# Kernel optimization log

Measured on AMD Instinct MI355X. Metric: run time of the kernel, lower is better.

The kernel has to match this reference:

```python
import jax, jax.numpy as jnp
import numpy as np

MASK_PROPORTION = 0.5
NEG_BIG = -99999999.0


def setup_inputs() -> dict:
    key = jax.random.key(0)
    k_x, k_w1, k_b1, k_w2, k_b2 = jax.random.split(key, 5)
    B, T, D, H = 32, 4096, 1024, 256
    x = jax.random.normal(k_x, (B, T, D), dtype=jnp.float32)
    s1 = 1.0 / np.sqrt(D)
    s2 = 1.0 / np.sqrt(H)
    W1 = jax.random.uniform(k_w1, (D, H), minval=-s1, maxval=s1, dtype=jnp.float32)
    b1 = jax.random.uniform(k_b1, (H,), minval=-s1, maxval=s1, dtype=jnp.float32)
    W2 = jax.random.uniform(k_w2, (H, 1), minval=-s2, maxval=s2, dtype=jnp.float32)
    b2 = jax.random.uniform(k_b2, (1,), minval=-s2, maxval=s2, dtype=jnp.float32)
    return {"x": x, "W1": W1, "b1": b1, "W2": W2, "b2": b2}


def reference(x, W1, b1, W2, b2):
    # e: [B, T, 1] attention scores from small MLP
    h = jnp.tanh(jnp.einsum("btd,dh->bth", x, W1) + b1)
    e = jnp.einsum("bth,ho->bto", h, W2) + b2  # [B, T, 1]

    T = e.shape[1]
    threshold_index = int(T * MASK_PROPORTION)
    sorted_e = jnp.sort(e, axis=1)
    threshold_value = sorted_e[:, threshold_index]          # [B, 1]
    # mask: +1 where e < threshold (kept), NEG_BIG where e >= threshold
    mask = jnp.where(e >= threshold_value[:, None, :], NEG_BIG, 1.0)
    e = e + mask
    beta = jax.nn.softmax(e, axis=1)                        # [B, T, 1]
    # bmm(beta^T, x) -> [B, 1, D], permute -> [B, D, 1], unsqueeze -> [B, D, 1, 1]
    out = jnp.einsum("bto,btd->bd", beta, x)
    return out[:, :, None, None]
```

## Files before the change

kernel.cpp:

```cpp
#include <hip/hip_runtime.h>
#include <hip/hip_bf16.h>
#include <math.h>

#define B_   32
#define T_   4096
#define D_   1024
#define H_   256
#define KTH  2048
#define SC   32
#define BM   128
#define BKE  32
#define NTE  (D_/BKE)
#define ABUF (BM*BKE)
#define BBUF (H_*BKE)
#define EPSB 4.0e-3f
#define MAXBAND 256
#define RB   4

typedef __attribute__((ext_vector_type(8))) short short8;
typedef __attribute__((ext_vector_type(4))) float f32x4;

#define FENCE4() asm volatile("s_waitcnt vmcnt(4) lgkmcnt(0)" ::: "memory")
#define FENCE0() asm volatile("s_waitcnt vmcnt(0) lgkmcnt(0)" ::: "memory")
#define BARRIER() __builtin_amdgcn_s_barrier()
#define SCHED()  __builtin_amdgcn_sched_barrier(0)
#define GLL(src, dst) __builtin_amdgcn_global_load_lds( \
    (const __attribute__((address_space(1))) unsigned int*)(src), \
    (__attribute__((address_space(3))) unsigned int*)(dst), 16, 0, 0)

__device__ inline unsigned f2s(float f) {
    unsigned u = __float_as_uint(f);
    return (u & 0x80000000u) ? ~u : (u | 0x80000000u);
}
__device__ inline float s2f(unsigned s) {
    unsigned x = (s & 0x80000000u) ? (s & 0x7fffffffu) : ~s;
    return __uint_as_float(x);
}
__device__ inline unsigned f2bf_rne(float f) {
    unsigned u = __float_as_uint(f);
    return (u + 0x7FFFu + ((u >> 16) & 1u)) >> 16;
}
__device__ inline unsigned pk2(float a, float b) {
    return f2bf_rne(a) | (f2bf_rne(b) << 16);
}
__device__ inline int block_sum_i(int v, int* sb, int tid) {
    #pragma unroll
    for (int o = 32; o; o >>= 1) v += __shfl_down(v, o);
    __syncthreads();
    if ((tid & 63) == 0) sb[tid >> 6] = v;
    __syncthreads();
    return sb[0] + sb[1] + sb[2] + sb[3];
}
__device__ inline float block_max_f(float v, float* sb, int tid) {
    #pragma unroll
    for (int o = 32; o; o >>= 1) v = fmaxf(v, __shfl_down(v, o));
    __syncthreads();
    if ((tid & 63) == 0) sb[tid >> 6] = v;
    __syncthreads();
    return fmaxf(fmaxf(sb[0], sb[1]), fmaxf(sb[2], sb[3]));
}
__device__ inline float block_sum_f(float v, float* sb, int tid) {
    #pragma unroll
    for (int o = 32; o; o >>= 1) v += __shfl_down(v, o);
    __syncthreads();
    if ((tid & 63) == 0) sb[tid >> 6] = v;
    __syncthreads();
    return sb[0] + sb[1] + sb[2] + sb[3];
}

__global__ __launch_bounds__(256) void k_w1t(const float* __restrict__ W1,
                                             ushort* __restrict__ Whi) {
    __shared__ float tile[32][33];
    const int kb = blockIdx.x * 32, nb = blockIdx.y * 32;
    const int tx = threadIdx.x & 31, ty = threadIdx.x >> 5;
    #pragma unroll
    for (int i = 0; i < 4; i++)
        tile[ty + 8*i][tx] = W1[(long)(kb + ty + 8*i) * H_ + nb + tx];
    __syncthreads();
    #pragma unroll
    for (int i = 0; i < 4; i++) {
        long o = (long)(nb + ty + 8*i) * D_ + kb + tx;
        Whi[o] = (ushort)f2bf_rne(tile[tx][ty + 8*i]);
    }
}

__global__ __launch_bounds__(512, 4) void k_e_mfma(
    const float* __restrict__ x,
    const ushort* __restrict__ Whi,
    const float* __restrict__ b1, const float* __restrict__ W2,
    const float* __restrict__ b2, float* __restrict__ e_out)
{
    __shared__ ushort sA[2][ABUF];
    __shared__ ushort sB[3][BBUF];
    __shared__ float  sRed[4][BM];

    const int tid  = threadIdx.x;
    const int lane = tid & 63;
    const int wv   = tid >> 6;
    const int wm   = wv >> 2, wn = wv & 3;
    const int l15  = lane & 15, lg = lane >> 4;
    const long row0 = (long)blockIdx.x * BM;

    const int ar = tid >> 2, aj = tid & 3;
    const float* aga = x + (row0 + ar) * (long)D_ + aj * 8;
    const int awo = (ar >> 4) * 512 + aj * 128 + (ar & 15) * 8;

    const int c0 = tid, c1 = tid + 512;
    const int bn0 = (c0 >> 6) * 16 + (c0 & 15), bk0 = (c0 >> 4) & 3;
    const int bn1 = (c1 >> 6) * 16 + (c1 & 15), bk1 = (c1 >> 4) & 3;
    const ushort* bga0 = Whi + (long)bn0 * D_ + bk0 * 8;
    const ushort* bga1 = Whi + (long)bn1 * D_ + bk1 * 8;
    const int bdst0 = c0 * 8, bdst1 = c1 * 8;

    int aoff[4], boff[4];
    #pragma unroll
    for (int fm = 0; fm < 4; fm++)
        aoff[fm] = (wm * 4 + fm) * 512 + lg * 128 + l15 * 8;
    #pragma unroll
    for (int fn = 0; fn < 4; fn++)
        boff[fn] = (wn * 4 + fn) * 512 + lg * 128 + l15 * 8;

    f32x4 acc[4][4];
    #pragma unroll
    for (int i = 0; i < 4; i++)
        #pragma unroll
        for (int j = 0; j < 4; j++) acc[i][j] = (f32x4){0.f, 0.f, 0.f, 0.f};

    ushort* sBb = (ushort*)sB;
    auto stageB = [&](int ko, int bi) {
        GLL(bga0 + ko, sBb + bi * BBUF + bdst0);
        GLL(bga1 + ko, sBb + bi * BBUF + bdst1);
    };
    auto writeA = [&](ushort* dst, const float4& a0, const float4& a1) {
        uint4 ap = make_uint4(pk2(a0.x, a0.y), pk2(a0.z, a0.w),
                              pk2(a1.x, a1.y), pk2(a1.z, a1.w));
        *(uint4*)&dst[awo] = ap;
    };
    auto compute = [&](const ushort* sa, const ushort* sb) {
        short8 bfr[4];
        #pragma unroll
        for (int fn = 0; fn < 4; fn++)
            bfr[fn] = *(const short8*)&sb[boff[fn]];
        #pragma unroll
        for (int fm = 0; fm < 4; fm++) {
            short8 afr = *(const short8*)&sa[aoff[fm]];
            #pragma unroll
            for (int fn = 0; fn < 4; fn++)
                acc[fm][fn] = __builtin_amdgcn_mfma_f32_16x16x32_bf16(afr, bfr[fn], acc[fm][fn], 0, 0, 0);
        }
    };

    float4 rA0a = *(const float4*)(aga);
    float4 rA0b = *(const float4*)(aga + 4);
    stageB(0, 0);
    float4 rA1a = *(const float4*)(aga + BKE);
    float4 rA1b = *(const float4*)(aga + BKE + 4);
    stageB(BKE, 1);
    writeA(sA[0], rA0a, rA0b);
    FENCE0(); BARRIER();

    for (int t = 0; t < NTE - 2; t += 2) {
        FENCE4(); BARRIER(); SCHED();
        {
            const int ko = (t + 2) * BKE;
            rA0a = *(const float4*)(aga + ko);
            rA0b = *(const float4*)(aga + ko + 4);
            stageB(ko, (t + 2) % 3);
            compute(sA[0], sBb + (t % 3) * BBUF);
            writeA(sA[1], rA1a, rA1b);
        }
        FENCE4(); BARRIER(); SCHED();
        {
            const int ko = (t + 3) * BKE;
            rA1a = *(const float4*)(aga + ko);
            rA1b = *(const float4*)(aga + ko + 4);
            stageB(ko, (t + 3) % 3);
            compute(sA[1], sBb + ((t + 1) % 3) * BBUF);
            writeA(sA[0], rA0a, rA0b);
        }
    }
    FENCE4(); BARRIER(); SCHED();
    compute(sA[0], sBb + ((NTE - 2) % 3) * BBUF);
    writeA(sA[1], rA1a, rA1b);
    FENCE0(); BARRIER(); SCHED();
    compute(sA[1], sBb + ((NTE - 1) % 3) * BBUF);

    float b1v[4], w2v[4];
    #pragma unroll
    for (int fn = 0; fn < 4; fn++) {
        int j = wn * 64 + fn * 16 + l15;
        b1v[fn] = b1[j]; w2v[fn] = W2[j];
    }
    #pragma unroll
    for (int fm = 0; fm < 4; fm++) {
        #pragma unroll
        for (int r = 0; r < 4; r++) {
            float s = 0.f;
            #pragma unroll
            for (int fn = 0; fn < 4; fn++)
                s += tanhf(acc[fm][fn][r] + b1v[fn]) * w2v[fn];
            s += __shfl_xor(s, 1); s += __shfl_xor(s, 2);
            s += __shfl_xor(s, 4); s += __shfl_xor(s, 8);
            if (l15 == 0) sRed[wn][wm * 64 + fm * 16 + lg * 4 + r] = s;
        }
    }
    __syncthreads();
    if (tid < BM)
        e_out[row0 + tid] = sRed[0][tid] + sRed[1][tid] + sRed[2][tid] + sRed[3][tid] + b2[0];
}

template<int BUILD>
__global__ __launch_bounds__(256) void k_thresh(const float* __restrict__ e,
                                                int* __restrict__ counts,
                                                int* __restrict__ list,
                                                int* __restrict__ sidx,
                                                float* __restrict__ sval,
                                                int* __restrict__ scount) {
    __shared__ int   sbi[4];
    __shared__ float sbf[4];
    __shared__ int   wsum[4];
    __shared__ int   scnt;
    const int b = blockIdx.x, tid = threadIdx.x;
    const int lane = tid & 63, wid = tid >> 6;
    const float* eb = e + (long)b * T_;
    const int t0 = tid * 16;

    float fe[16]; unsigned ue[16];
    #pragma unroll
    for (int i = 0; i < 16; i += 4) {
        float4 v = *(const float4*)(eb + t0 + i);
        fe[i] = v.x; fe[i+1] = v.y; fe[i+2] = v.z; fe[i+3] = v.w;
    }
    #pragma unroll
    for (int i = 0; i < 16; i++) ue[i] = f2s(fe[i]);

    unsigned lo = 0u, hi = 0xFFFFFFFFu;
    while (lo < hi) {
        unsigned mid = lo + ((hi - lo) >> 1);
        int c = 0;
        #pragma unroll
        for (int i = 0; i < 16; i++) c += (ue[i] <= mid) ? 1 : 0;
        int total = block_sum_i(c, sbi, tid);
        if (total >= KTH + 1) hi = mid; else lo = mid + 1;
    }
    const float thr = s2f(lo);

    if (BUILD) {
        if (tid == 0) scnt = 0;
        __syncthreads();
        #pragma unroll
        for (int i = 0; i < 16; i++) {
            if (fabsf(fe[i] - thr) <= EPSB) {
                int p = atomicAdd(&scnt, 1);
                if (p < MAXBAND) list[b * MAXBAND + p] = t0 + i;
            }
        }
        __syncthreads();
        if (tid == 0) counts[b] = scnt < MAXBAND ? scnt : MAXBAND;
    } else {
        float m = -INFINITY;
        #pragma unroll
        for (int i = 0; i < 16; i++) if (fe[i] < thr) m = fmaxf(m, fe[i]);
        m = block_max_f(m, sbf, tid);
        float s = 0.f;
        #pragma unroll
        for (int i = 0; i < 16; i++) if (fe[i] < thr) s += expf(fe[i] - m);
        s = block_sum_f(s, sbf, tid);
        const float inv = 1.0f / s;

        int c = 0;
        #pragma unroll
        for (int i = 0; i < 16; i++) c += (fe[i] < thr) ? 1 : 0;
        int p = c;
        #pragma unroll
        for (int o = 1; o < 64; o <<= 1) {
            int y = __shfl_up(p, o);
            if (lane >= o) p += y;
        }
        if (lane == 63) wsum[wid] = p;
        __syncthreads();
        int base = 0;
        #pragma unroll
        for (int w = 0; w < 4; w++) base += (w < wid) ? wsum[w] : 0;
        int pos = base + p - c;
        #pragma unroll
        for (int i = 0; i < 16; i++) {
            if (fe[i] < thr) {
                sidx[(long)b * T_ + pos] = t0 + i;
                sval[(long)b * T_ + pos] = expf(fe[i] - m) * inv;
                pos++;
            }
        }
        if (tid == 0) scount[b] = wsum[0] + wsum[1] + wsum[2] + wsum[3];
    }
}

__global__ __launch_bounds__(256) void k_refine(const float* __restrict__ x,
        const float* __restrict__ W1, const float* __restrict__ b1,
        const float* __restrict__ W2, const float* __restrict__ b2,
        const int* __restrict__ counts, const int* __restrict__ list,
        float* __restrict__ e) {
    const int b   = blockIdx.y;
    const int blk = blockIdx.x;
    const int cnt = counts[b];
    const int tid = threadIdx.x;
    __shared__ float xs[RB][D_];
    __shared__ float sbf[4];

    for (int g = blk * RB; g < cnt; g += 16 * RB) {
        const int nr = min(RB, cnt - g);
        for (int j = 0; j < nr; j++) {
            const int t = list[b * MAXBAND + g + j];
            *(float4*)&xs[j][tid * 4] =
                *(const float4*)&x[((long)b * T_ + t) * D_ + tid * 4];
        }
        __syncthreads();

        float a0 = 0.f, a1 = 0.f, a2 = 0.f, a3 = 0.f;
        for (int k0 = 0; k0 < D_; k0 += 4) {
            const float w0 = W1[(long)(k0 + 0) * H_ + tid];
            const float w1v = W1[(long)(k0 + 1) * H_ + tid];
            const float w2q = W1[(long)(k0 + 2) * H_ + tid];
            const float w3 = W1[(long)(k0 + 3) * H_ + tid];
            {
                float4 xv = *(const float4*)&xs[0][k0];
                a0 = fmaf(xv.x, w0, a0); a0 = fmaf(xv.y, w1v, a0);
                a0 = fmaf(xv.z, w2q, a0); a0 = fmaf(xv.w, w3, a0);
            }
            {
                float4 xv = *(const float4*)&xs[1][k0];
                a1 = fmaf(xv.x, w0, a1); a1 = fmaf(xv.y, w1v, a1);
                a1 = fmaf(xv.z, w2q, a1); a1 = fmaf(xv.w, w3, a1);
            }
            {
                float4 xv = *(const float4*)&xs[2][k0];
                a2 = fmaf(xv.x, w0, a2); a2 = fmaf(xv.y, w1v, a2);
                a2 = fmaf(xv.z, w2q, a2); a2 = fmaf(xv.w, w3, a2);
            }
            {
                float4 xv = *(const float4*)&xs[3][k0];
                a3 = fmaf(xv.x, w0, a3); a3 = fmaf(xv.y, w1v, a3);
                a3 = fmaf(xv.z, w2q, a3); a3 = fmaf(xv.w, w3, a3);
            }
        }

        float aj[RB] = {a0, a1, a2, a3};
        for (int j = 0; j < nr; j++) {
            float v = tanhf(aj[j] + b1[tid]) * W2[tid];
            float tot = block_sum_f(v, sbf, tid);
            if (tid == 0) {
                const int t = list[b * MAXBAND + g + j];
                e[(long)b * T_ + t] = tot + b2[0];
            }
            __syncthreads();
        }
        __syncthreads();
    }
}

__global__ __launch_bounds__(256) void k_pv(const float* __restrict__ x,
                                            const int* __restrict__ sidx,
                                            const float* __restrict__ sval,
                                            const int* __restrict__ scount,
                                            float* __restrict__ partial) {
    const int c = blockIdx.x, b = blockIdx.y, tid = threadIdx.x;
    const int cnt = scount[b];
    const int len = (cnt + SC - 1) / SC;
    const int k0 = c * len;
    const int nl = min(len, cnt - k0);
    __shared__ int   si[96];
    __shared__ float sv[96];
    if (tid < nl) {
        si[tid] = sidx[(long)b * T_ + k0 + tid];
        sv[tid] = sval[(long)b * T_ + k0 + tid];
    }
    __syncthreads();

    float4 acc = {0.f, 0.f, 0.f, 0.f};
    const float* xb = x + (long)b * T_ * D_ + tid * 4;
    for (int k = 0; k < nl; k++) {
        const float w = sv[k];
        float4 v = *(const float4*)(xb + (long)si[k] * D_);
        acc.x = fmaf(w, v.x, acc.x);
        acc.y = fmaf(w, v.y, acc.y);
        acc.z = fmaf(w, v.z, acc.z);
        acc.w = fmaf(w, v.w, acc.w);
    }
    *(float4*)&partial[(((long)b * SC) + c) * D_ + tid * 4] = acc;
}

__global__ __launch_bounds__(256) void k_red(const float* __restrict__ partial,
                                             float* __restrict__ out) {
    const int b = blockIdx.x, tid = threadIdx.x;
    float4 acc = {0.f, 0.f, 0.f, 0.f};
    #pragma unroll
    for (int c = 0; c < SC; c++) {
        float4 v = *(const float4*)&partial[(((long)b * SC) + c) * D_ + tid * 4];
        acc.x += v.x; acc.y += v.y; acc.z += v.z; acc.w += v.w;
    }
    *(float4*)&out[(long)b * D_ + tid * 4] = acc;
}

extern "C" void kernel_launch(void* const* d_in, const int* in_sizes, int n_in,
                              void* d_out, int out_size, void* d_ws, size_t ws_size,
                              hipStream_t stream) {
    const float* x  = (const float*)d_in[0];
    const float* W1 = (const float*)d_in[1];
    const float* b1 = (const float*)d_in[2];
    const float* W2 = (const float*)d_in[3];
    const float* b2 = (const float*)d_in[4];
    float* out = (float*)d_out;

    char* ws = (char*)d_ws;
    float* e       = (float*)ws;  ws += (size_t)B_ * T_ * 4;
    int*   sidx    = (int*)ws;    ws += (size_t)B_ * T_ * 4;
    float* sval    = (float*)ws;  ws += (size_t)B_ * T_ * 4;
    float* partial = (float*)ws;  ws += (size_t)B_ * SC * D_ * 4;
    ushort* Whi    = (ushort*)ws; ws += (size_t)H_ * D_ * 2;
    int* counts    = (int*)ws;    ws += 128;
    int* scountp   = (int*)ws;    ws += 128;
    int* list      = (int*)ws;

    k_w1t<<<dim3(D_ / 32, H_ / 32), 256, 0, stream>>>(W1, Whi);
    k_e_mfma<<<(B_ * T_) / BM, 512, 0, stream>>>(x, Whi, b1, W2, b2, e);
    k_thresh<1><<<B_, 256, 0, stream>>>(e, counts, list, sidx, sval, scountp);
    k_refine<<<dim3(16, B_), 256, 0, stream>>>(x, W1, b1, W2, b2, counts, list, e);
    k_thresh<0><<<B_, 256, 0, stream>>>(e, counts, list, sidx, sval, scountp);
    k_pv<<<dim3(SC, B_), 256, 0, stream>>>(x, sidx, sval, scountp, partial);
    k_red<<<B_, 256, 0, stream>>>(partial, out);
}
```

Baseline: 319.3 us.

## Restructure e-score GEMM into 256-row tiles with 4-phase ping-pong pipeline

Result: slower. 368.5 us (+15.4%).

```diff
diff --git a/kernel.cpp b/kernel.cpp
--- a/kernel.cpp
+++ b/kernel.cpp
@@ -8,11 +8,8 @@
 #define H_   256
 #define KTH  2048
 #define SC   32
-#define BM   128
-#define BKE  32
-#define NTE  (D_/BKE)
-#define ABUF (BM*BKE)
-#define BBUF (H_*BKE)
+#define BKL  64
+#define NKT  (D_/BKL)
 #define EPSB 4.0e-3f
 #define MAXBAND 256
 #define RB   4
@@ -20,10 +17,8 @@
 typedef __attribute__((ext_vector_type(8))) short short8;
 typedef __attribute__((ext_vector_type(4))) float f32x4;
 
-#define FENCE4() asm volatile("s_waitcnt vmcnt(4) lgkmcnt(0)" ::: "memory")
 #define FENCE0() asm volatile("s_waitcnt vmcnt(0) lgkmcnt(0)" ::: "memory")
 #define BARRIER() __builtin_amdgcn_s_barrier()
-#define SCHED()  __builtin_amdgcn_sched_barrier(0)
 #define GLL(src, dst) __builtin_amdgcn_global_load_lds( \
     (const __attribute__((address_space(1))) unsigned int*)(src), \
     (__attribute__((address_space(3))) unsigned int*)(dst), 16, 0, 0)
@@ -84,106 +79,135 @@
     }
 }
 
-__global__ __launch_bounds__(512, 4) void k_e_mfma(
+__global__ __launch_bounds__(512, 2) void k_e_mfma(
     const float* __restrict__ x,
     const ushort* __restrict__ Whi,
     const float* __restrict__ b1, const float* __restrict__ W2,
     const float* __restrict__ b2, float* __restrict__ e_out)
 {
-    __shared__ ushort sA[2][ABUF];
-    __shared__ ushort sB[3][BBUF];
-    __shared__ float  sRed[4][BM];
+    __shared__ ushort smem[65536];
 
     const int tid  = threadIdx.x;
     const int lane = tid & 63;
     const int wv   = tid >> 6;
     const int wm   = wv >> 2, wn = wv & 3;
     const int l15  = lane & 15, lg = lane >> 4;
-    const long row0 = (long)blockIdx.x * BM;
-
-    const int ar = tid >> 2, aj = tid & 3;
-    const float* aga = x + (row0 + ar) * (long)D_ + aj * 8;
-    const int awo = (ar >> 4) * 512 + aj * 128 + (ar & 15) * 8;
-
-    const int c0 = tid, c1 = tid + 512;
-    const int bn0 = (c0 >> 6) * 16 + (c0 & 15), bk0 = (c0 >> 4) & 3;
-    const int bn1 = (c1 >> 6) * 16 + (c1 & 15), bk1 = (c1 >> 4) & 3;
-    const ushort* bga0 = Whi + (long)bn0 * D_ + bk0 * 8;
-    const ushort* bga1 = Whi + (long)bn1 * D_ + bk1 * 8;
-    const int bdst0 = c0 * 8, bdst1 = c1 * 8;
-
-    int aoff[4], boff[4];
-    #pragma unroll
-    for (int fm = 0; fm < 4; fm++)
-        aoff[fm] = (wm * 4 + fm) * 512 + lg * 128 + l15 * 8;
-    #pragma unroll
-    for (int fn = 0; fn < 4; fn++)
-        boff[fn] = (wn * 4 + fn) * 512 + lg * 128 + l15 * 8;
-
-    f32x4 acc[4][4];
-    #pragma unroll
-    for (int i = 0; i < 4; i++)
+    const long row0 = (long)blockIdx.x * 256;
+
+    ushort* sA0 = smem;
+    ushort* sA1 = smem + 16384;
+    ushort* sB0 = smem + 32768;
+    ushort* sB1 = smem + 49152;
+
+    const int ar = tid >> 1, ah = tid & 1;
+    const float* aga = x + (row0 + ar) * (long)D_ + ah * 32;
+    const int awo = (ar >> 4) * 1024 + (ar & 15) * 8;
+
+    const ushort* bsrc[4]; int bdst[4];
+    #pragma unroll
+    for (int j = 0; j < 4; j++) {
+        const int c = tid + j * 512;
+        const int slab = c >> 7, kc = (c >> 4) & 7, row = c & 15;
+        bsrc[j] = Whi + (long)(slab * 16 + row) * D_ + kc * 8;
+        bdst[j] = c * 8;
+    }
+
+    const int abase = wm * 8192 + lg * 128 + l15 * 8;
+    const int bbase = wn * 4096 + lg * 128 + l15 * 8;
+
+    f32x4 acc[8][4];
+    #pragma unroll
+    for (int i = 0; i < 8; i++)
         #pragma unroll
         for (int j = 0; j < 4; j++) acc[i][j] = (f32x4){0.f, 0.f, 0.f, 0.f};
 
-    ushort* sBb = (ushort*)sB;
-    auto stageB = [&](int ko, int bi) {
-        GLL(bga0 + ko, sBb + bi * BBUF + bdst0);
-        GLL(bga1 + ko, sBb + bi * BBUF + bdst1);
-    };
-    auto writeA = [&](ushort* dst, const float4& a0, const float4& a1) {
-        uint4 ap = make_uint4(pk2(a0.x, a0.y), pk2(a0.z, a0.w),
-                              pk2(a1.x, a1.y), pk2(a1.z, a1.w));
-        *(uint4*)&dst[awo] = ap;
-    };
-    auto compute = [&](const ushort* sa, const ushort* sb) {
-        short8 bfr[4];
-        #pragma unroll
-        for (int fn = 0; fn < 4; fn++)
-            bfr[fn] = *(const short8*)&sb[boff[fn]];
-        #pragma unroll
-        for (int fm = 0; fm < 4; fm++) {
-            short8 afr = *(const short8*)&sa[aoff[fm]];
-            #pragma unroll
-            for (int fn = 0; fn < 4; fn++)
-                acc[fm][fn] = __builtin_amdgcn_mfma_f32_16x16x32_bf16(afr, bfr[fn], acc[fm][fn], 0, 0, 0);
-        }
-    };
-
-    float4 rA0a = *(const float4*)(aga);
-    float4 rA0b = *(const float4*)(aga + 4);
-    stageB(0, 0);
-    float4 rA1a = *(const float4*)(aga + BKE);
-    float4 rA1b = *(const float4*)(aga + BKE + 4);
-    stageB(BKE, 1);
-    writeA(sA[0], rA0a, rA0b);
-    FENCE0(); BARRIER();
-
-    for (int t = 0; t < NTE - 2; t += 2) {
-        FENCE4(); BARRIER(); SCHED();
-        {
-            const int ko = (t + 2) * BKE;
-            rA0a = *(const float4*)(aga + ko);
-            rA0b = *(const float4*)(aga + ko + 4);
-            stageB(ko, (t + 2) % 3);
-            compute(sA[0], sBb + (t % 3) * BBUF);
-            writeA(sA[1], rA1a, rA1b);
-        }
-        FENCE4(); BARRIER(); SCHED();
-        {
-            const int ko = (t + 3) * BKE;
-            rA1a = *(const float4*)(aga + ko);
-            rA1b = *(const float4*)(aga + ko + 4);
-            stageB(ko, (t + 3) % 3);
-            compute(sA[1], sBb + ((t + 1) % 3) * BBUF);
-            writeA(sA[0], rA0a, rA0b);
-        }
-    }
-    FENCE4(); BARRIER(); SCHED();
-    compute(sA[0], sBb + ((NTE - 2) % 3) * BBUF);
-    writeA(sA[1], rA1a, rA1b);
-    FENCE0(); BARRIER(); SCHED();
-    compute(sA[1], sBb + ((NTE - 1) % 3) * BBUF);
+    float4 Ra[8];
+
+#define LOADS_A() do { if (more) { \
+    _Pragma("unroll") \
+    for (int q = 0; q < 8; q++) Ra[q] = *(const float4*)(aga + ko + q * 4); \
+} } while (0)
+#define GLL01() do { if (more) { \
+    GLL(bsrc[0] + ko, sBn + bdst[0]); \
+    GLL(bsrc[1] + ko, sBn + bdst[1]); \
+} } while (0)
+#define GLL23() do { if (more) { \
+    GLL(bsrc[2] + ko, sBn + bdst[2]); \
+    GLL(bsrc[3] + ko, sBn + bdst[3]); \
+} } while (0)
+#define AWRITE() do { if (more) { \
+    _Pragma("unroll") \
+    for (int q = 0; q < 4; q++) { \
+        uint4 _u = make_uint4(pk2(Ra[2*q].x, Ra[2*q].y), pk2(Ra[2*q].z, Ra[2*q].w), \
+                              pk2(Ra[2*q+1].x, Ra[2*q+1].y), pk2(Ra[2*q+1].z, Ra[2*q+1].w)); \
+        *(uint4*)&sAn[awo + (ah * 4 + q) * 128] = _u; \
+    } \
+} } while (0)
+#define NOOP() do {} while (0)
+
+#define PHASE(MH, NH, STAGE_STMT, FENCE_STMT) do { \
+    short8 _af[2][4], _bf[2][2]; \
+    _Pragma("unroll") \
+    for (int kh = 0; kh < 2; kh++) { \
+        _Pragma("unroll") \
+        for (int fm = 0; fm < 4; fm++) \
+            _af[kh][fm] = *(const short8*)&sAc[abase + ((MH)*4 + fm) * 1024 + kh * 512]; \
+        _Pragma("unroll") \
+        for (int fn = 0; fn < 2; fn++) \
+            _bf[kh][fn] = *(const short8*)&sBc[bbase + ((NH)*2 + fn) * 1024 + kh * 512]; \
+    } \
+    STAGE_STMT; \
+    BARRIER(); \
+    asm volatile("s_waitcnt lgkmcnt(0)" ::: "memory"); \
+    __builtin_amdgcn_sched_barrier(0); \
+    __builtin_amdgcn_s_setprio(1); \
+    _Pragma("unroll") \
+    for (int kh = 0; kh < 2; kh++) \
+        _Pragma("unroll") \
+        for (int fm = 0; fm < 4; fm++) \
+            _Pragma("unroll") \
+            for (int fn = 0; fn < 2; fn++) \
+                acc[(MH)*4 + fm][(NH)*2 + fn] = __builtin_amdgcn_mfma_f32_16x16x32_bf16( \
+                    _af[kh][fm], _bf[kh][fn], acc[(MH)*4 + fm][(NH)*2 + fn], 0, 0, 0); \
+    __builtin_amdgcn_s_setprio(0); \
+    FENCE_STMT; \
+    BARRIER(); \
+} while (0)
+
+    {
+        #pragma unroll
+        for (int j = 0; j < 4; j++) GLL(bsrc[j], sB0 + bdst[j]);
+        #pragma unroll
+        for (int q = 0; q < 8; q++) Ra[q] = *(const float4*)(aga + q * 4);
+        #pragma unroll
+        for (int q = 0; q < 4; q++) {
+            uint4 u = make_uint4(pk2(Ra[2*q].x, Ra[2*q].y), pk2(Ra[2*q].z, Ra[2*q].w),
+                                 pk2(Ra[2*q+1].x, Ra[2*q+1].y), pk2(Ra[2*q+1].z, Ra[2*q+1].w));
+            *(uint4*)&sA0[awo + (ah * 4 + q) * 128] = u;
+        }
+        FENCE0(); BARRIER();
+    }
+
+    for (int t = 0; t < NKT; ++t) {
+        const ushort* sAc = (t & 1) ? sA1 : sA0;
+        const ushort* sBc = (t & 1) ? sB1 : sB0;
+        ushort* sAn = (t & 1) ? sA0 : sA1;
+        ushort* sBn = (t & 1) ? sB0 : sB1;
+        const bool more = (t + 1 < NKT);
+        const int ko = (t + 1) * BKL;
+
+        PHASE(0, 0, LOADS_A(), NOOP());
+        PHASE(0, 1, GLL01(),   NOOP());
+        PHASE(1, 0, GLL23(),   NOOP());
+        PHASE(1, 1, AWRITE(),  FENCE0());
+    }
+
+#undef PHASE
+#undef NOOP
+#undef AWRITE
+#undef GLL23
+#undef GLL01
+#undef LOADS_A
 
     float b1v[4], w2v[4];
     #pragma unroll
@@ -191,8 +215,9 @@
         int j = wn * 64 + fn * 16 + l15;
         b1v[fn] = b1[j]; w2v[fn] = W2[j];
     }
-    #pragma unroll
-    for (int fm = 0; fm < 4; fm++) {
+    float* sRed = (float*)smem;
+    #pragma unroll
+    for (int fm = 0; fm < 8; fm++) {
         #pragma unroll
         for (int r = 0; r < 4; r++) {
             float s = 0.f;
@@ -201,12 +226,12 @@
                 s += tanhf(acc[fm][fn][r] + b1v[fn]) * w2v[fn];
             s += __shfl_xor(s, 1); s += __shfl_xor(s, 2);
             s += __shfl_xor(s, 4); s += __shfl_xor(s, 8);
-            if (l15 == 0) sRed[wn][wm * 64 + fm * 16 + lg * 4 + r] = s;
-        }
-    }
-    __syncthreads();
-    if (tid < BM)
-        e_out[row0 + tid] = sRed[0][tid] + sRed[1][tid] + sRed[2][tid] + sRed[3][tid] + b2[0];
+            if (l15 == 0) sRed[wn * 256 + wm * 128 + fm * 16 + lg * 4 + r] = s;
+        }
+    }
+    __syncthreads();
+    if (tid < 256)
+        e_out[row0 + tid] = sRed[tid] + sRed[256 + tid] + sRed[512 + tid] + sRed[768 + tid] + b2[0];
 }
 
 template<int BUILD>
@@ -422,7 +447,7 @@
     int* list      = (int*)ws;
 
     k_w1t<<<dim3(D_ / 32, H_ / 32), 256, 0, stream>>>(W1, Whi);
-    k_e_mfma<<<(B_ * T_) / BM, 512, 0, stream>>>(x, Whi, b1, W2, b2, e);
+    k_e_mfma<<<(B_ * T_) / 256, 512, 0, stream>>>(x, Whi, b1, W2, b2, e);
     k_thresh<1><<<B_, 256, 0, stream>>>(e, counts, list, sidx, sval, scountp);
     k_refine<<<dim3(16, B_), 256, 0, stream>>>(x, W1, b1, W2, b2, counts, list, e);
     k_thresh<0><<<B_, 256, 0, stream>>>(e, counts, list, sidx, sval, scountp);
```
